# Kernel optimization log

Measured on AMD Instinct MI355X. Metric: run time of the kernel, lower is better.

Reference implementation:

```python
import jax, jax.numpy as jnp
import numpy as np

E, K = 8, 2            # num_experts, top_k
H, DFF = 1024, 2048    # embd_dim, d_ff
B, S = 4, 1024


def setup_inputs() -> dict:
    key = jax.random.key(0)
    ks = jax.random.split(key, 5)
    s_in = 1.0 / np.sqrt(H)
    s_ff = 1.0 / np.sqrt(DFF)
    return {
        "x": jax.random.normal(ks[0], (B, S, H), jnp.float32),
        "centroids": jax.random.normal(ks[1], (E, H), jnp.float32),
        # nn.Linear weights are [out, in]
        "gate_w": jax.random.normal(ks[2], (E, DFF, H), jnp.float32) * s_in,
        "up_w": jax.random.normal(ks[3], (E, DFF, H), jnp.float32) * s_in,
        "down_w": jax.random.normal(ks[4], (E, H, DFF), jnp.float32) * s_ff,
        "routing_bias": jnp.zeros((E,), jnp.float32),
    }


def reference(x, centroids, gate_w, up_w, down_w, routing_bias):
    Bb, Ss, Hh = x.shape
    xf = x.reshape(-1, Hh)  # [T, H]
    # sigmoid affinity router + (non-trainable) routing bias
    affinity = jax.nn.sigmoid(xf @ centroids.T)          # [T, E]
    topk_scores, topk_idx = jax.lax.top_k(affinity + routing_bias, K)  # [T, K]
    topk_w = jax.nn.softmax(topk_scores, axis=-1)        # [T, K]

    # Dense per-expert SwiGLU FFN on all tokens (same math as the
    # sort/gather grouped loop; selection happens in the gather below).
    g = jnp.einsum('th,efh->etf', xf, gate_w)            # [E, T, DFF]
    u = jnp.einsum('th,efh->etf', xf, up_w)              # [E, T, DFF]
    y = jnp.einsum('etf,ehf->eth', jax.nn.silu(g) * u, down_w)  # [E, T, H]

    yt = jnp.transpose(y, (1, 0, 2))                     # [T, E, H]
    sel = jnp.take_along_axis(yt, topk_idx[:, :, None], axis=1)  # [T, K, H]
    out_flat = jnp.sum(sel * topk_w[:, :, None], axis=1)  # [T, H]

    counts = jnp.bincount(topk_idx.ravel(), length=E)    # per-expert token counts
    return out_flat.reshape(Bb, Ss, Hh), counts
```

## Files before the change

kernel.cpp:

```cpp
#include <hip/hip_runtime.h>
#include <math.h>

constexpr int E = 8, H = 1024, DFF = 2048, T = 4096;
constexpr int TR = 8192;
constexpr int MAXJ = 72;

typedef __bf16 bf16x8 __attribute__((ext_vector_type(8)));
typedef __bf16 bf16x4 __attribute__((ext_vector_type(4)));
typedef float f32x4 __attribute__((ext_vector_type(4)));

__device__ __forceinline__ void gload16(const void* g, void* l) {
    __builtin_amdgcn_global_load_lds(
        (const __attribute__((address_space(1))) unsigned int*)g,
        (__attribute__((address_space(3))) unsigned int*)l, 16, 0, 0);
}

constexpr int CONV_BLOCKS = 3072;
__global__ __launch_bounds__(256) void k0_fused(
    const float* __restrict__ x, const float* __restrict__ cent,
    const float* __restrict__ bias,
    int* __restrict__ se, float* __restrict__ sw,
    const float* __restrict__ gw, __bf16* __restrict__ gwb,
    const float* __restrict__ uw, __bf16* __restrict__ uwb,
    __bf16* __restrict__ xb, int w4, int x4, int* __restrict__ done) {
    __shared__ float cs[E * H];
    int tid = threadIdx.x;

    if (blockIdx.x == 0 && tid == 0) *done = 0;

    if (blockIdx.x >= 1024) {
        int total = 2 * w4 + x4;
        int stride = CONV_BLOCKS * 256;
        for (int i = (blockIdx.x - 1024) * 256 + tid; i < total; i += stride) {
            const float* in; __bf16* outp; int idx;
            if (i < w4) { in = gw; outp = gwb; idx = i; }
            else if (i < 2 * w4) { in = uw; outp = uwb; idx = i - w4; }
            else { in = x; outp = xb; idx = i - 2 * w4; }
            float4 v = ((const float4*)in)[idx];
            bf16x4 o = {(__bf16)v.x, (__bf16)v.y, (__bf16)v.z, (__bf16)v.w};
            ((bf16x4*)outp)[idx] = o;
        }
        return;
    }

    for (int i = tid; i < E * H / 4; i += 256)
        ((float4*)cs)[i] = ((const float4*)cent)[i];
    __syncthreads();

    int wave = tid >> 6, lane = tid & 63;
    int t = blockIdx.x * 4 + wave;
    const float4* xr = (const float4*)(x + (size_t)t * H);
    float acc[E] = {};
    #pragma unroll
    for (int it = 0; it < 4; it++) {
        float4 xv = xr[lane + it * 64];
        #pragma unroll
        for (int e = 0; e < E; e++) {
            float4 cv = ((const float4*)(cs + e * H))[lane + it * 64];
            acc[e] = fmaf(xv.x, cv.x, acc[e]);
            acc[e] = fmaf(xv.y, cv.y, acc[e]);
            acc[e] = fmaf(xv.z, cv.z, acc[e]);
            acc[e] = fmaf(xv.w, cv.w, acc[e]);
        }
    }
    #pragma unroll
    for (int off = 32; off; off >>= 1)
        #pragma unroll
        for (int e = 0; e < E; e++) acc[e] += __shfl_down(acc[e], off);

    if (lane == 0) {
        float s[E];
        #pragma unroll
        for (int e = 0; e < E; e++)
            s[e] = 1.0f / (1.0f + expf(-acc[e])) + bias[e];
        int i0 = 0;
        for (int e = 1; e < E; e++) if (s[e] > s[i0]) i0 = e;
        int i1 = -1;
        for (int e = 0; e < E; e++) {
            if (e == i0) continue;
            if (i1 < 0 || s[e] > s[i1]) i1 = e;
        }
        float m = fmaxf(s[i0], s[i1]);
        float w0 = expf(s[i0] - m), w1 = expf(s[i1] - m);
        float inv = 1.0f / (w0 + w1);
        se[2 * t] = i0;     sw[2 * t] = w0 * inv;
        se[2 * t + 1] = i1; sw[2 * t + 1] = w1 * inv;
    }
}

__global__ __launch_bounds__(1024) void k1b_partition(
    const int* __restrict__ se, int* __restrict__ token_list,
    int* __restrict__ sp, int* __restrict__ cnt,
    int* __restrict__ off, float* __restrict__ out_counts,
    int* __restrict__ jobs, int* __restrict__ njobs, int* __restrict__ done) {
    int e = blockIdx.x;
    int tid = threadIdx.x;
    int wave = tid >> 6, lane = tid & 63;
    __shared__ int wsum[16];
    int running = 0;
    for (int c0 = 0; c0 < 2 * T; c0 += 1024) {
        int i = c0 + tid;
        bool pred = (se[i] == e);
        unsigned long long mask = __ballot(pred);
        int pos_in_wave = __popcll(mask & ((1ull << lane) - 1ull));
        if (lane == 0) wsum[wave] = __popcll(mask);
        __syncthreads();
        int wbase = 0;
        #pragma unroll
        for (int w2 = 0; w2 < 16; w2++) {
            int v = wsum[w2];
            if (w2 < wave) wbase += v;
        }
        int total = 0;
        #pragma unroll
        for (int w2 = 0; w2 < 16; w2++) total += wsum[w2];
        if (pred) {
            int p = running + wbase + pos_in_wave;
            token_list[e * T + p] = i >> 1;
            sp[i] = p;
        }
        running += total;
        __syncthreads();
    }
    if (tid == 0) {
        __hip_atomic_store(&cnt[e], running, __ATOMIC_RELEASE, __HIP_MEMORY_SCOPE_AGENT);
        int prev = __hip_atomic_fetch_add(done, 1, __ATOMIC_ACQ_REL, __HIP_MEMORY_SCOPE_AGENT);
        if (prev == E - 1) {
            int acc = 0, nj = 0;
            for (int e2 = 0; e2 < E; e2++) {
                int c = __hip_atomic_load(&cnt[e2], __ATOMIC_ACQUIRE, __HIP_MEMORY_SCOPE_AGENT);
                off[e2] = acc; acc += c;
                out_counts[e2] = (float)c;
                int mts = (c + 127) >> 7;
                for (int mt = 0; mt < mts; mt++) jobs[nj++] = e2 * 64 + mt;
            }
            njobs[0] = nj;
        }
    }
}

constexpr int KCONV_BLOCKS = 1024;
__global__ __launch_bounds__(256) void k_conv(const float* __restrict__ in,
                                              __bf16* __restrict__ out, int n4) {
    int stride = KCONV_BLOCKS * 256;
    for (int i = blockIdx.x * 256 + threadIdx.x; i < n4; i += stride) {
        float4 v = ((const float4*)in)[i];
        bf16x4 o = {(__bf16)v.x, (__bf16)v.y, (__bf16)v.z, (__bf16)v.w};
        ((bf16x4*)out)[i] = o;
    }
}

__global__ __launch_bounds__(256, 2) void k2_gateup(
    const __bf16* __restrict__ xb, const __bf16* __restrict__ gwb,
    const __bf16* __restrict__ uwb, const int* __restrict__ cnt,
    const int* __restrict__ off, const int* __restrict__ token_list,
    const int* __restrict__ jobs, const int* __restrict__ njobs,
    __bf16* __restrict__ h) {
    int jt = blockIdx.x >> 4, nt = blockIdx.x & 15;
    if (jt >= njobs[0]) return;
    int job = jobs[jt];
    int e = job >> 6, mt = job & 63;
    int Me = cnt[e], offe = off[e];

    __shared__ __bf16 As[128 * 64];
    __shared__ __bf16 Bg[128 * 64];
    __shared__ __bf16 Bu[128 * 64];

    int tid = threadIdx.x;
    int lane = tid & 63, w = tid >> 6;
    int wm = w >> 1, wn = w & 1;

    const __bf16* asrc[4];
    const __bf16 *bsg[4], *bsu[4];
    #pragma unroll
    for (int rr = 0; rr < 4; rr++) {
        int l = rr * 256 + tid;
        int row = l >> 3, sl = l & 7;
        int gr = mt * 128 + row; if (gr >= Me) gr = Me - 1;
        int tok = token_list[e * T + gr];
        asrc[rr] = xb + (size_t)tok * H + ((sl ^ (row & 7)) * 8);
        size_t base = ((size_t)e * DFF + nt * 128 + row) * H + ((sl ^ (row & 7)) * 8);
        bsg[rr] = gwb + base;
        bsu[rr] = uwb + base;
    }

    f32x4 accg[4][4] = {};
    f32x4 accu[4][4] = {};
    int kq = lane >> 4, m15 = lane & 15;

    for (int k0 = 0; k0 < H; k0 += 64) {
        #pragma unroll
        for (int rr = 0; rr < 4; rr++) {
            gload16(asrc[rr] + k0, &As[(rr * 256 + tid) * 8]);
            gload16(bsg[rr] + k0, &Bg[(rr * 256 + tid) * 8]);
            gload16(bsu[rr] + k0, &Bu[(rr * 256 + tid) * 8]);
        }
        __syncthreads();

        #pragma unroll
        for (int kc = 0; kc < 2; kc++) {
            bf16x8 af[4], gf[4], uf[4];
            #pragma unroll
            for (int i = 0; i < 4; i++) {
                int row = wm * 64 + i * 16 + m15;
                int sl = (kc * 4 + kq) ^ (row & 7);
                af[i] = *(const bf16x8*)&As[row * 64 + sl * 8];
            }
            #pragma unroll
            for (int j = 0; j < 4; j++) {
                int row = wn * 64 + j * 16 + m15;
                int sl = (kc * 4 + kq) ^ (row & 7);
                gf[j] = *(const bf16x8*)&Bg[row * 64 + sl * 8];
                uf[j] = *(const bf16x8*)&Bu[row * 64 + sl * 8];
            }
            #pragma unroll
            for (int i = 0; i < 4; i++)
                #pragma unroll
                for (int j = 0; j < 4; j++) {
                    accg[i][j] = __builtin_amdgcn_mfma_f32_16x16x32_bf16(af[i], gf[j], accg[i][j], 0, 0, 0);
                    accu[i][j] = __builtin_amdgcn_mfma_f32_16x16x32_bf16(af[i], uf[j], accu[i][j], 0, 0, 0);
                }
        }
        __syncthreads();
    }

    #pragma unroll
    for (int i = 0; i < 4; i++)
        #pragma unroll
        for (int j = 0; j < 4; j++) {
            int nloc = wn * 64 + j * 16 + m15;
            size_t c = (size_t)nt * 128 + nloc;
            #pragma unroll
            for (int p = 0; p < 4; p++) {
                int mloc = wm * 64 + i * 16 + kq * 4 + p;
                int mrow = mt * 128 + mloc;
                if (mrow < Me) {
                    float g = accg[i][j][p], u = accu[i][j][p];
                    float sig = 1.0f / (1.0f + __expf(-g));
                    h[(size_t)(offe + mrow) * DFF + c] = (__bf16)(g * sig * u);
                }
            }
        }
}

__global__ __launch_bounds__(256, 2) void k3_down(
    const __bf16* __restrict__ h, const __bf16* __restrict__ dwb,
    const int* __restrict__ cnt, const int* __restrict__ off,
    const int* __restrict__ jobs, const int* __restrict__ njobs,
    __bf16* __restrict__ y) {
    int jt = blockIdx.x >> 3, nt = blockIdx.x & 7;
    if (jt >= njobs[0]) return;
    int job = jobs[jt];
    int e = job >> 6, mt = job & 63;
    int Me = cnt[e], offe = off[e];

    __shared__ __bf16 As[128 * 64];
    __shared__ __bf16 Bs[128 * 64];

    int tid = threadIdx.x;
    int lane = tid & 63, w = tid >> 6;
    int wm = w >> 1, wn = w & 1;

    const __bf16* asrc[4];
    const __bf16* bsrc[4];
    #pragma unroll
    for (int rr = 0; rr < 4; rr++) {
        int l = rr * 256 + tid;
        int row = l >> 3, sl = l & 7;
        int koff = (sl ^ (row & 7)) * 8;
        int gr = mt * 128 + row; if (gr >= Me) gr = Me - 1;
        asrc[rr] = h + (size_t)(offe + gr) * DFF + koff;
        bsrc[rr] = dwb + ((size_t)e * H + nt * 128 + row) * DFF + koff;
    }

    f32x4 acc[4][4] = {};
    int kq = lane >> 4, m15 = lane & 15;

    for (int k0 = 0; k0 < DFF; k0 += 64) {
        #pragma unroll
        for (int rr = 0; rr < 4; rr++)
            gload16(asrc[rr] + k0, &As[(rr * 256 + tid) * 8]);
        #pragma unroll
        for (int rr = 0; rr < 4; rr++)
            gload16(bsrc[rr] + k0, &Bs[(rr * 256 + tid) * 8]);
        __syncthreads();

        #pragma unroll
        for (int kc = 0; kc < 2; kc++) {
            bf16x8 af[4], bf[4];
            #pragma unroll
            for (int i = 0; i < 4; i++) {
                int row = wm * 64 + i * 16 + m15;
                int sl = (kc * 4 + kq) ^ (row & 7);
                af[i] = *(const bf16x8*)&As[row * 64 + sl * 8];
            }
            #pragma unroll
            for (int j = 0; j < 4; j++) {
                int row = wn * 64 + j * 16 + m15;
                int sl = (kc * 4 + kq) ^ (row & 7);
                bf[j] = *(const bf16x8*)&Bs[row * 64 + sl * 8];
            }
            #pragma unroll
            for (int i = 0; i < 4; i++)
                #pragma unroll
                for (int j = 0; j < 4; j++)
                    acc[i][j] = __builtin_amdgcn_mfma_f32_16x16x32_bf16(af[i], bf[j], acc[i][j], 0, 0, 0);
        }
        __syncthreads();
    }

    #pragma unroll
    for (int i = 0; i < 4; i++)
        #pragma unroll
        for (int j = 0; j < 4; j++) {
            int nglob = nt * 128 + wn * 64 + j * 16 + m15;
            #pragma unroll
            for (int p = 0; p < 4; p++) {
                int mloc = wm * 64 + i * 16 + kq * 4 + p;
                int mrow = mt * 128 + mloc;
                if (mrow < Me)
                    y[(size_t)(offe + mrow) * H + nglob] = (__bf16)acc[i][j][p];
            }
        }
}

__global__ __launch_bounds__(256) void k_gather(
    const __bf16* __restrict__ y, const int* __restrict__ se,
    const int* __restrict__ sp, const float* __restrict__ sw,
    const int* __restrict__ off, float* __restrict__ out) {
    int t = blockIdx.x;
    int r0 = off[se[2 * t]] + sp[2 * t];
    int r1 = off[se[2 * t + 1]] + sp[2 * t + 1];
    float w0 = sw[2 * t], w1 = sw[2 * t + 1];
    const bf16x4* y0 = (const bf16x4*)(y + (size_t)r0 * H);
    const bf16x4* y1 = (const bf16x4*)(y + (size_t)r1 * H);
    float4* o = (float4*)(out + (size_t)t * H);
    int c = threadIdx.x;
    bf16x4 a = y0[c], b = y1[c];
    float4 v;
    v.x = w0 * (float)a[0] + w1 * (float)b[0];
    v.y = w0 * (float)a[1] + w1 * (float)b[1];
    v.z = w0 * (float)a[2] + w1 * (float)b[2];
    v.w = w0 * (float)a[3] + w1 * (float)b[3];
    o[c] = v;
}

extern "C" void kernel_launch(void* const* d_in, const int* in_sizes, int n_in,
                              void* d_out, int out_size, void* d_ws, size_t ws_size,
                              hipStream_t stream) {
    const float* x    = (const float*)d_in[0];
    const float* cent = (const float*)d_in[1];
    const float* gw   = (const float*)d_in[2];
    const float* uw   = (const float*)d_in[3];
    const float* dw   = (const float*)d_in[4];
    const float* bias = (const float*)d_in[5];
    float* out = (float*)d_out;

    char* ws = (char*)d_ws;
    int*   cnt        = (int*)(ws + 0);
    int*   off        = (int*)(ws + 64);
    int*   se         = (int*)(ws + 128);
    int*   sp         = (int*)(ws + 128 + 32768);
    float* sw         = (float*)(ws + 128 + 65536);
    int*   token_list = (int*)(ws + 128 + 98304);
    int*   jobs       = (int*)(ws + 229504);
    int*   njobs      = (int*)(ws + 229824);
    int*   done       = (int*)(ws + 229888);
    const size_t MB = 1u << 20;
    __bf16* gwb = (__bf16*)(ws + 1 * MB);
    __bf16* uwb = (__bf16*)(ws + 1 * MB + 33554432);
    __bf16* dwb = gwb;
    __bf16* y   = uwb;
    __bf16* xb  = (__bf16*)(ws + 1 * MB + 67108864);
    __bf16* h   = (__bf16*)(ws + 1 * MB + 75497472);

    const int W4 = E * DFF * H / 4;
    const int X4 = T * H / 4;

    k0_fused<<<1024 + CONV_BLOCKS, 256, 0, stream>>>(
        x, cent, bias, se, sw, gw, gwb, uw, uwb, xb, W4, X4, done);
    k1b_partition<<<E, 1024, 0, stream>>>(se, token_list, sp, cnt,
                                          off, out + (size_t)T * H, jobs, njobs, done);
    k2_gateup<<<MAXJ * 16, 256, 0, stream>>>(xb, gwb, uwb, cnt, off, token_list, jobs, njobs, h);
    k_conv<<<KCONV_BLOCKS, 256, 0, stream>>>(dw, dwb, W4);
    k3_down<<<MAXJ * 8, 256, 0, stream>>>(h, dwb, cnt, off, jobs, njobs, y);
    k_gather<<<T, 256, 0, stream>>>(y, se, sp, sw, off, out);
}
```

Before: 381.8 us.

## Rewrite gate/up GEMM as 256-row tile with double-buffered phased pipeline

The gate/up kernel moves from 128x128 tiles with 256 threads and a single-buffered load/sync loop to 256-row M tiles with 512 threads (8 waves). It uses double-buffered LDS, split into eight phases per iteration that overlap global-to-LDS loads with MFMA work, and adds explicit waitcnt, barriers and setprio scheduling. The partition kernel now emits a separate job list for this tiling while the down kernel keeps 128-row jobs. The aim is to hide memory latency and raise reuse of the weight tiles across more rows. The cost is about 128KB of LDS per block, more padded work for partially filled experts, and fragile hand-tuned vmcnt accounting.

Result: slower. 398.8 us (+4.4%).

```diff
diff --git a/kernel.cpp b/kernel.cpp
--- a/kernel.cpp
+++ b/kernel.cpp
@@ -3,7 +3,8 @@
 
 constexpr int E = 8, H = 1024, DFF = 2048, T = 4096;
 constexpr int TR = 8192;
-constexpr int MAXJ = 72;
+constexpr int MAXJ2 = TR / 256 + E;
+constexpr int MAXJ3 = TR / 128 + E;
 
 typedef __bf16 bf16x8 __attribute__((ext_vector_type(8)));
 typedef __bf16 bf16x4 __attribute__((ext_vector_type(4)));
@@ -92,7 +93,8 @@
     const int* __restrict__ se, int* __restrict__ token_list,
     int* __restrict__ sp, int* __restrict__ cnt,
     int* __restrict__ off, float* __restrict__ out_counts,
-    int* __restrict__ jobs, int* __restrict__ njobs, int* __restrict__ done) {
+    int* __restrict__ jobs2, int* __restrict__ jobs3,
+    int* __restrict__ njobs, int* __restrict__ done) {
     int e = blockIdx.x;
     int tid = threadIdx.x;
     int wave = tid >> 6, lane = tid & 63;
@@ -126,15 +128,18 @@
         __hip_atomic_store(&cnt[e], running, __ATOMIC_RELEASE, __HIP_MEMORY_SCOPE_AGENT);
         int prev = __hip_atomic_fetch_add(done, 1, __ATOMIC_ACQ_REL, __HIP_MEMORY_SCOPE_AGENT);
         if (prev == E - 1) {
-            int acc = 0, nj = 0;
+            int acc = 0, nj2 = 0, nj3 = 0;
             for (int e2 = 0; e2 < E; e2++) {
                 int c = __hip_atomic_load(&cnt[e2], __ATOMIC_ACQUIRE, __HIP_MEMORY_SCOPE_AGENT);
                 off[e2] = acc; acc += c;
                 out_counts[e2] = (float)c;
-                int mts = (c + 127) >> 7;
-                for (int mt = 0; mt < mts; mt++) jobs[nj++] = e2 * 64 + mt;
+                int m2 = (c + 255) >> 8;
+                for (int mt = 0; mt < m2; mt++) jobs2[nj2++] = e2 * 64 + mt;
+                int m3 = (c + 127) >> 7;
+                for (int mt = 0; mt < m3; mt++) jobs3[nj3++] = e2 * 64 + mt;
             }
-            njobs[0] = nj;
+            njobs[0] = nj2;
+            njobs[1] = nj3;
         }
     }
 }
@@ -150,90 +155,137 @@
     }
 }
 
-__global__ __launch_bounds__(256, 2) void k2_gateup(
+__global__ __launch_bounds__(512, 2) void k2_gateup(
     const __bf16* __restrict__ xb, const __bf16* __restrict__ gwb,
     const __bf16* __restrict__ uwb, const int* __restrict__ cnt,
     const int* __restrict__ off, const int* __restrict__ token_list,
-    const int* __restrict__ jobs, const int* __restrict__ njobs,
+    const int* __restrict__ jobs2, const int* __restrict__ njobs,
     __bf16* __restrict__ h) {
     int jt = blockIdx.x >> 4, nt = blockIdx.x & 15;
     if (jt >= njobs[0]) return;
-    int job = jobs[jt];
+    int job = jobs2[jt];
     int e = job >> 6, mt = job & 63;
     int Me = cnt[e], offe = off[e];
 
-    __shared__ __bf16 As[128 * 64];
-    __shared__ __bf16 Bg[128 * 64];
-    __shared__ __bf16 Bu[128 * 64];
+    __shared__ __bf16 smA[2][16384];
+    __shared__ __bf16 smB[2][16384];
 
     int tid = threadIdx.x;
     int lane = tid & 63, w = tid >> 6;
-    int wm = w >> 1, wn = w & 1;
-
-    const __bf16* asrc[4];
-    const __bf16 *bsg[4], *bsu[4];
+    int wm = w >> 2, wn = w & 3;
+    int kq = lane >> 4, m15 = lane & 15;
+
+    const __bf16 *aptr00, *aptr01, *aptr10, *aptr11;
+    const __bf16 *bptr00, *bptr01, *bptr10, *bptr11;
+    {
+        int l20 = tid,       rl0 = l20 >> 3, ch0 = (l20 & 7) ^ (rl0 & 7);
+        int l21 = 512 + tid, rl1 = l21 >> 3, ch1 = (l21 & 7) ^ (rl1 & 7);
+        int g00 = mt * 256 + rl0;       if (g00 >= Me) g00 = Me - 1;
+        int g01 = mt * 256 + rl1;       if (g01 >= Me) g01 = Me - 1;
+        int g10 = mt * 256 + 128 + rl0; if (g10 >= Me) g10 = Me - 1;
+        int g11 = mt * 256 + 128 + rl1; if (g11 >= Me) g11 = Me - 1;
+        aptr00 = xb + (size_t)token_list[e * T + g00] * H + ch0 * 8;
+        aptr01 = xb + (size_t)token_list[e * T + g01] * H + ch1 * 8;
+        aptr10 = xb + (size_t)token_list[e * T + g10] * H + ch0 * 8;
+        aptr11 = xb + (size_t)token_list[e * T + g11] * H + ch1 * 8;
+        size_t wb0 = ((size_t)e * DFF + nt * 128 + rl0) * H + ch0 * 8;
+        size_t wb1 = ((size_t)e * DFF + nt * 128 + rl1) * H + ch1 * 8;
+        bptr00 = gwb + wb0; bptr01 = gwb + wb1;
+        bptr10 = uwb + wb0; bptr11 = uwb + wb1;
+    }
+
+#define STAGE_A0(KK, BUF) { gload16(aptr00 + (KK)*64, &smA[BUF][tid*8]); \
+                            gload16(aptr01 + (KK)*64, &smA[BUF][4096 + tid*8]); }
+#define STAGE_A1(KK, BUF) { gload16(aptr10 + (KK)*64, &smA[BUF][8192 + tid*8]); \
+                            gload16(aptr11 + (KK)*64, &smA[BUF][8192 + 4096 + tid*8]); }
+#define STAGE_B0(KK, BUF) { gload16(bptr00 + (KK)*64, &smB[BUF][tid*8]); \
+                            gload16(bptr01 + (KK)*64, &smB[BUF][4096 + tid*8]); }
+#define STAGE_B1(KK, BUF) { gload16(bptr10 + (KK)*64, &smB[BUF][8192 + tid*8]); \
+                            gload16(bptr11 + (KK)*64, &smB[BUF][8192 + 4096 + tid*8]); }
+
+    int slb0 = ((0 + kq) ^ (m15 & 7)) * 8;
+    int slb1 = ((4 + kq) ^ (m15 & 7)) * 8;
+    int arow = wm * 64 + m15;
+    int brow = wn * 32 + m15;
+
+    f32x4 accg[8][2] = {};
+    f32x4 accu[8][2] = {};
+    bf16x8 af[4], gf[2], uf[2];
+
+#define LDA4(BUF, IH, SLB) { \
+    af[0] = *(const bf16x8*)&smA[BUF][(arow + (IH)*128 +  0)*64 + (SLB)]; \
+    af[1] = *(const bf16x8*)&smA[BUF][(arow + (IH)*128 + 16)*64 + (SLB)]; \
+    af[2] = *(const bf16x8*)&smA[BUF][(arow + (IH)*128 + 32)*64 + (SLB)]; \
+    af[3] = *(const bf16x8*)&smA[BUF][(arow + (IH)*128 + 48)*64 + (SLB)]; }
+#define LDB4(BUF, SLB) { \
+    gf[0] = *(const bf16x8*)&smB[BUF][(brow +   0)*64 + (SLB)]; \
+    gf[1] = *(const bf16x8*)&smB[BUF][(brow +  16)*64 + (SLB)]; \
+    uf[0] = *(const bf16x8*)&smB[BUF][(brow + 128)*64 + (SLB)]; \
+    uf[1] = *(const bf16x8*)&smB[BUF][(brow + 144)*64 + (SLB)]; }
+#define MFMA16(IH) { \
+    _Pragma("unroll") \
+    for (int i2 = 0; i2 < 4; i2++) { \
+        _Pragma("unroll") \
+        for (int j = 0; j < 2; j++) { \
+            accg[(IH)*4 + i2][j] = __builtin_amdgcn_mfma_f32_16x16x32_bf16(af[i2], gf[j], accg[(IH)*4 + i2][j], 0, 0, 0); \
+            accu[(IH)*4 + i2][j] = __builtin_amdgcn_mfma_f32_16x16x32_bf16(af[i2], uf[j], accu[(IH)*4 + i2][j], 0, 0, 0); \
+        } } }
+#define PH_SYNC  { __builtin_amdgcn_s_barrier(); \
+                   asm volatile("s_waitcnt lgkmcnt(0)" ::: "memory"); \
+                   __builtin_amdgcn_sched_barrier(0); \
+                   __builtin_amdgcn_s_setprio(1); }
+#define PH_ENDVM { __builtin_amdgcn_s_setprio(0); \
+                   asm volatile("s_waitcnt vmcnt(4)" ::: "memory"); \
+                   __builtin_amdgcn_s_barrier(); }
+#define PH_END   { __builtin_amdgcn_s_setprio(0); \
+                   __builtin_amdgcn_s_barrier(); }
+
+    STAGE_A0(0, 0); STAGE_B0(0, 0); STAGE_B1(0, 0); STAGE_A1(0, 0);
+    STAGE_A0(1, 1);
+    asm volatile("s_waitcnt vmcnt(4)" ::: "memory");
+    __builtin_amdgcn_s_barrier();
+
+    for (int i = 0; i < 8; ++i) {
+        int kb  = 2 * i + 1;
+        int ka2 = (2 * i + 2) & 15;
+        int kb2 = (2 * i + 3) & 15;
+
+        LDA4(0, 0, slb0); LDB4(0, slb0);
+        STAGE_B0(kb, 1);
+        PH_SYNC; MFMA16(0); PH_ENDVM;
+        LDA4(0, 1, slb0);
+        STAGE_B1(kb, 1);
+        PH_SYNC; MFMA16(1); PH_END;
+        LDA4(0, 0, slb1); LDB4(0, slb1);
+        STAGE_A1(kb, 1);
+        PH_SYNC; MFMA16(0); PH_END;
+        LDA4(0, 1, slb1);
+        STAGE_A0(ka2, 0);
+        PH_SYNC; MFMA16(1); PH_ENDVM;
+        LDA4(1, 0, slb0); LDB4(1, slb0);
+        STAGE_B0(ka2, 0);
+        PH_SYNC; MFMA16(0); PH_ENDVM;
+        LDA4(1, 1, slb0);
+        STAGE_B1(ka2, 0);
+        PH_SYNC; MFMA16(1); PH_END;
+        LDA4(1, 0, slb1); LDB4(1, slb1);
+        STAGE_A1(ka2, 0);
+        PH_SYNC; MFMA16(0); PH_END;
+        LDA4(1, 1, slb1);
+        STAGE_A0(kb2, 1);
+        PH_SYNC; MFMA16(1); PH_ENDVM;
+    }
+
     #pragma unroll
-    for (int rr = 0; rr < 4; rr++) {
-        int l = rr * 256 + tid;
-        int row = l >> 3, sl = l & 7;
-        int gr = mt * 128 + row; if (gr >= Me) gr = Me - 1;
-        int tok = token_list[e * T + gr];
-        asrc[rr] = xb + (size_t)tok * H + ((sl ^ (row & 7)) * 8);
-        size_t base = ((size_t)e * DFF + nt * 128 + row) * H + ((sl ^ (row & 7)) * 8);
-        bsg[rr] = gwb + base;
-        bsu[rr] = uwb + base;
-    }
-
-    f32x4 accg[4][4] = {};
-    f32x4 accu[4][4] = {};
-    int kq = lane >> 4, m15 = lane & 15;
-
-    for (int k0 = 0; k0 < H; k0 += 64) {
-        #pragma unroll
-        for (int rr = 0; rr < 4; rr++) {
-            gload16(asrc[rr] + k0, &As[(rr * 256 + tid) * 8]);
-            gload16(bsg[rr] + k0, &Bg[(rr * 256 + tid) * 8]);
-            gload16(bsu[rr] + k0, &Bu[(rr * 256 + tid) * 8]);
-        }
-        __syncthreads();
-
-        #pragma unroll
-        for (int kc = 0; kc < 2; kc++) {
-            bf16x8 af[4], gf[4], uf[4];
-            #pragma unroll
-            for (int i = 0; i < 4; i++) {
-                int row = wm * 64 + i * 16 + m15;
-                int sl = (kc * 4 + kq) ^ (row & 7);
-                af[i] = *(const bf16x8*)&As[row * 64 + sl * 8];
-            }
-            #pragma unroll
-            for (int j = 0; j < 4; j++) {
-                int row = wn * 64 + j * 16 + m15;
-                int sl = (kc * 4 + kq) ^ (row & 7);
-                gf[j] = *(const bf16x8*)&Bg[row * 64 + sl * 8];
-                uf[j] = *(const bf16x8*)&Bu[row * 64 + sl * 8];
-            }
-            #pragma unroll
-            for (int i = 0; i < 4; i++)
-                #pragma unroll
-                for (int j = 0; j < 4; j++) {
-                    accg[i][j] = __builtin_amdgcn_mfma_f32_16x16x32_bf16(af[i], gf[j], accg[i][j], 0, 0, 0);
-                    accu[i][j] = __builtin_amdgcn_mfma_f32_16x16x32_bf16(af[i], uf[j], accu[i][j], 0, 0, 0);
-                }
-        }
-        __syncthreads();
-    }
-
-    #pragma unroll
-    for (int i = 0; i < 4; i++)
-        #pragma unroll
-        for (int j = 0; j < 4; j++) {
-            int nloc = wn * 64 + j * 16 + m15;
-            size_t c = (size_t)nt * 128 + nloc;
+    for (int i = 0; i < 8; i++) {
+        int ih = i >> 2, i2 = i & 3;
+        #pragma unroll
+        for (int j = 0; j < 2; j++) {
+            int c = nt * 128 + wn * 32 + j * 16 + m15;
             #pragma unroll
             for (int p = 0; p < 4; p++) {
-                int mloc = wm * 64 + i * 16 + kq * 4 + p;
-                int mrow = mt * 128 + mloc;
+                int mloc = ih * 128 + wm * 64 + i2 * 16 + kq * 4 + p;
+                int mrow = mt * 256 + mloc;
                 if (mrow < Me) {
                     float g = accg[i][j][p], u = accu[i][j][p];
                     float sig = 1.0f / (1.0f + __expf(-g));
@@ -241,16 +293,27 @@
                 }
             }
         }
+    }
+#undef STAGE_A0
+#undef STAGE_A1
+#undef STAGE_B0
+#undef STAGE_B1
+#undef LDA4
+#undef LDB4
+#undef MFMA16
+#undef PH_SYNC
+#undef PH_ENDVM
+#undef PH_END
 }
 
 __global__ __launch_bounds__(256, 2) void k3_down(
     const __bf16* __restrict__ h, const __bf16* __restrict__ dwb,
     const int* __restrict__ cnt, const int* __restrict__ off,
-    const int* __restrict__ jobs, const int* __restrict__ njobs,
+    const int* __restrict__ jobs3, const int* __restrict__ njobs,
     __bf16* __restrict__ y) {
     int jt = blockIdx.x >> 3, nt = blockIdx.x & 7;
-    if (jt >= njobs[0]) return;
-    int job = jobs[jt];
+    if (jt >= njobs[1]) return;
+    int job = jobs3[jt];
     int e = job >> 6, mt = job & 63;
     int Me = cnt[e], offe = off[e];
 
@@ -363,9 +426,10 @@
     int*   sp         = (int*)(ws + 128 + 32768);
     float* sw         = (float*)(ws + 128 + 65536);
     int*   token_list = (int*)(ws + 128 + 98304);
-    int*   jobs       = (int*)(ws + 229504);
-    int*   njobs      = (int*)(ws + 229824);
-    int*   done       = (int*)(ws + 229888);
+    int*   jobs2      = (int*)(ws + 229504);
+    int*   jobs3      = (int*)(ws + 229760);
+    int*   njobs      = (int*)(ws + 230144);
+    int*   done       = (int*)(ws + 230208);
     const size_t MB = 1u << 20;
     __bf16* gwb = (__bf16*)(ws + 1 * MB);
     __bf16* uwb = (__bf16*)(ws + 1 * MB + 33554432);
@@ -380,9 +444,9 @@
     k0_fused<<<1024 + CONV_BLOCKS, 256, 0, stream>>>(
         x, cent, bias, se, sw, gw, gwb, uw, uwb, xb, W4, X4, done);
     k1b_partition<<<E, 1024, 0, stream>>>(se, token_list, sp, cnt,
-                                          off, out + (size_t)T * H, jobs, njobs, done);
-    k2_gateup<<<MAXJ * 16, 256, 0, stream>>>(xb, gwb, uwb, cnt, off, token_list, jobs, njobs, h);
+                                          off, out + (size_t)T * H, jobs2, jobs3, njobs, done);
+    k2_gateup<<<MAXJ2 * 16, 512, 0, stream>>>(xb, gwb, uwb, cnt, off, token_list, jobs2, njobs, h);
     k_conv<<<KCONV_BLOCKS, 256, 0, stream>>>(dw, dwb, W4);
-    k3_down<<<MAXJ * 8, 256, 0, stream>>>(h, dwb, cnt, off, jobs, njobs, y);
+    k3_down<<<MAXJ3 * 8, 256, 0, stream>>>(h, dwb, cnt, off, jobs3, njobs, y);
     k_gather<<<T, 256, 0, stream>>>(y, se, sp, sw, off, out);
 }
```

## Fuse weighted combine into down-projection epilogue with atomic adds

Applied to the files above, without the earlier changes.

The separate gather kernel and bf16 intermediate y buffer are removed. The down-projection epilogue now scales each row by its routing weight and atomically adds into the fp32 output, indexed through the token list. The output is zeroed inside the first kernel's conversion blocks. This saves a kernel launch and the y round trip, at the cost of scattered fp32 atomics (two per output element) and a nondeterministic summation order.

New measurement: 392.9 us. 1.03x slower.

```diff
diff --git a/kernel.cpp b/kernel.cpp
--- a/kernel.cpp
+++ b/kernel.cpp
@@ -22,16 +22,22 @@
     int* __restrict__ se, float* __restrict__ sw,
     const float* __restrict__ gw, __bf16* __restrict__ gwb,
     const float* __restrict__ uw, __bf16* __restrict__ uwb,
-    __bf16* __restrict__ xb, int w4, int x4, int* __restrict__ done) {
+    __bf16* __restrict__ xb, float* __restrict__ outz,
+    int w4, int x4, int o4, int* __restrict__ done) {
     __shared__ float cs[E * H];
     int tid = threadIdx.x;
 
     if (blockIdx.x == 0 && tid == 0) *done = 0;
 
     if (blockIdx.x >= 1024) {
-        int total = 2 * w4 + x4;
+        int total = 2 * w4 + x4 + o4;
         int stride = CONV_BLOCKS * 256;
         for (int i = (blockIdx.x - 1024) * 256 + tid; i < total; i += stride) {
+            if (i >= 2 * w4 + x4) {
+                float4 z = {0.f, 0.f, 0.f, 0.f};
+                ((float4*)outz)[i - 2 * w4 - x4] = z;
+                continue;
+            }
             const float* in; __bf16* outp; int idx;
             if (i < w4) { in = gw; outp = gwb; idx = i; }
             else if (i < 2 * w4) { in = uw; outp = uwb; idx = i - w4; }
@@ -89,8 +95,9 @@
 }
 
 __global__ __launch_bounds__(1024) void k1b_partition(
-    const int* __restrict__ se, int* __restrict__ token_list,
-    int* __restrict__ sp, int* __restrict__ cnt,
+    const int* __restrict__ se, const float* __restrict__ sw,
+    int* __restrict__ token_list, float* __restrict__ wlist,
+    int* __restrict__ cnt,
     int* __restrict__ off, float* __restrict__ out_counts,
     int* __restrict__ jobs, int* __restrict__ njobs, int* __restrict__ done) {
     int e = blockIdx.x;
@@ -117,7 +124,7 @@
         if (pred) {
             int p = running + wbase + pos_in_wave;
             token_list[e * T + p] = i >> 1;
-            sp[i] = p;
+            wlist[e * T + p] = sw[i];
         }
         running += total;
         __syncthreads();
@@ -246,8 +253,9 @@
 __global__ __launch_bounds__(256, 2) void k3_down(
     const __bf16* __restrict__ h, const __bf16* __restrict__ dwb,
     const int* __restrict__ cnt, const int* __restrict__ off,
+    const int* __restrict__ token_list, const float* __restrict__ wlist,
     const int* __restrict__ jobs, const int* __restrict__ njobs,
-    __bf16* __restrict__ y) {
+    float* __restrict__ out) {
     int jt = blockIdx.x >> 3, nt = blockIdx.x & 7;
     if (jt >= njobs[0]) return;
     int job = jobs[jt];
@@ -310,39 +318,23 @@
     }
 
     #pragma unroll
-    for (int i = 0; i < 4; i++)
-        #pragma unroll
-        for (int j = 0; j < 4; j++) {
-            int nglob = nt * 128 + wn * 64 + j * 16 + m15;
-            #pragma unroll
-            for (int p = 0; p < 4; p++) {
-                int mloc = wm * 64 + i * 16 + kq * 4 + p;
-                int mrow = mt * 128 + mloc;
-                if (mrow < Me)
-                    y[(size_t)(offe + mrow) * H + nglob] = (__bf16)acc[i][j][p];
-            }
-        }
-}
-
-__global__ __launch_bounds__(256) void k_gather(
-    const __bf16* __restrict__ y, const int* __restrict__ se,
-    const int* __restrict__ sp, const float* __restrict__ sw,
-    const int* __restrict__ off, float* __restrict__ out) {
-    int t = blockIdx.x;
-    int r0 = off[se[2 * t]] + sp[2 * t];
-    int r1 = off[se[2 * t + 1]] + sp[2 * t + 1];
-    float w0 = sw[2 * t], w1 = sw[2 * t + 1];
-    const bf16x4* y0 = (const bf16x4*)(y + (size_t)r0 * H);
-    const bf16x4* y1 = (const bf16x4*)(y + (size_t)r1 * H);
-    float4* o = (float4*)(out + (size_t)t * H);
-    int c = threadIdx.x;
-    bf16x4 a = y0[c], b = y1[c];
-    float4 v;
-    v.x = w0 * (float)a[0] + w1 * (float)b[0];
-    v.y = w0 * (float)a[1] + w1 * (float)b[1];
-    v.z = w0 * (float)a[2] + w1 * (float)b[2];
-    v.w = w0 * (float)a[3] + w1 * (float)b[3];
-    o[c] = v;
+    for (int i = 0; i < 4; i++) {
+        #pragma unroll
+        for (int p = 0; p < 4; p++) {
+            int mloc = wm * 64 + i * 16 + kq * 4 + p;
+            int mrow = mt * 128 + mloc;
+            if (mrow < Me) {
+                int tok = token_list[e * T + mrow];
+                float wgt = wlist[e * T + mrow];
+                float* orow = out + (size_t)tok * H;
+                #pragma unroll
+                for (int j = 0; j < 4; j++) {
+                    int nglob = nt * 128 + wn * 64 + j * 16 + m15;
+                    atomicAdd(&orow[nglob], wgt * acc[i][j][p]);
+                }
+            }
+        }
+    }
 }
 
 extern "C" void kernel_launch(void* const* d_in, const int* in_sizes, int n_in,
@@ -360,29 +352,28 @@
     int*   cnt        = (int*)(ws + 0);
     int*   off        = (int*)(ws + 64);
     int*   se         = (int*)(ws + 128);
-    int*   sp         = (int*)(ws + 128 + 32768);
-    float* sw         = (float*)(ws + 128 + 65536);
-    int*   token_list = (int*)(ws + 128 + 98304);
-    int*   jobs       = (int*)(ws + 229504);
-    int*   njobs      = (int*)(ws + 229824);
-    int*   done       = (int*)(ws + 229888);
+    float* sw         = (float*)(ws + 128 + 32768);
+    int*   token_list = (int*)(ws + 128 + 65536);
+    float* wlist      = (float*)(ws + 128 + 196608);
+    int*   jobs       = (int*)(ws + 327808);
+    int*   njobs      = (int*)(ws + 328128);
+    int*   done       = (int*)(ws + 328192);
     const size_t MB = 1u << 20;
     __bf16* gwb = (__bf16*)(ws + 1 * MB);
     __bf16* uwb = (__bf16*)(ws + 1 * MB + 33554432);
     __bf16* dwb = gwb;
-    __bf16* y   = uwb;
     __bf16* xb  = (__bf16*)(ws + 1 * MB + 67108864);
     __bf16* h   = (__bf16*)(ws + 1 * MB + 75497472);
 
     const int W4 = E * DFF * H / 4;
     const int X4 = T * H / 4;
+    const int O4 = T * H / 4;
 
     k0_fused<<<1024 + CONV_BLOCKS, 256, 0, stream>>>(
-        x, cent, bias, se, sw, gw, gwb, uw, uwb, xb, W4, X4, done);
-    k1b_partition<<<E, 1024, 0, stream>>>(se, token_list, sp, cnt,
+        x, cent, bias, se, sw, gw, gwb, uw, uwb, xb, out, W4, X4, O4, done);
+    k1b_partition<<<E, 1024, 0, stream>>>(se, sw, token_list, wlist, cnt,
                                           off, out + (size_t)T * H, jobs, njobs, done);
     k2_gateup<<<MAXJ * 16, 256, 0, stream>>>(xb, gwb, uwb, cnt, off, token_list, jobs, njobs, h);
     k_conv<<<KCONV_BLOCKS, 256, 0, stream>>>(dw, dwb, W4);
-    k3_down<<<MAXJ * 8, 256, 0, stream>>>(h, dwb, cnt, off, jobs, njobs, y);
-    k_gather<<<T, 256, 0, stream>>>(y, se, sp, sw, off, out);
-}
+    k3_down<<<MAXJ * 8, 256, 0, stream>>>(h, dwb, cnt, off, token_list, wlist, jobs, njobs, out);
+}
```
